# Kernel tuning notes

Measured on AMD Instinct MI355X. Metric: run time of the kernel, lower is better.

## Reference

```python
import jax, jax.numpy as jnp
import numpy as np

B, D_IN, D_HID, NH, PF = 1024, 2048, 4096, 8, 2
D_UP = D_IN * PF          # 4096
HS = D_HID // NH          # 512 head size
EPS = 1e-5


def setup_inputs() -> dict:
    key = jax.random.key(0)
    ks = jax.random.split(key, 24)
    it = iter(range(24))

    def lin(k, fin, fout):
        # weight stored as (in, out); y = x @ W + b
        return jax.random.normal(k, (fin, fout), jnp.float32) / np.float32(np.sqrt(fin))

    def bd(k, fin_blk, fout_blk):
        # block-diagonal per-head weights (NH, in_blk, out_blk)
        return jax.random.normal(k, (NH, fin_blk, fout_blk), jnp.float32) / np.float32(np.sqrt(fin_blk))

    inp = {}
    inp['x'] = jax.random.normal(ks[next(it)], (B, D_IN), jnp.float32)
    inp['h_prev'] = jax.random.normal(ks[next(it)], (B, D_HID), jnp.float32)
    inp['c_prev'] = jax.random.normal(ks[next(it)], (B, D_HID), jnp.float32)
    inp['n_prev'] = jax.random.normal(ks[next(it)], (B, D_HID), jnp.float32)
    inp['m_prev'] = jax.random.normal(ks[next(it)], (B, D_HID), jnp.float32)
    inp['ln_w'] = jnp.ones((D_IN,), jnp.float32)
    inp['ln_b'] = jnp.zeros((D_IN,), jnp.float32)
    inp['upL_w'] = lin(ks[next(it)], D_IN, D_UP); inp['upL_b'] = jnp.zeros((D_UP,), jnp.float32)
    inp['upR_w'] = lin(ks[next(it)], D_IN, D_HID); inp['upR_b'] = jnp.zeros((D_HID,), jnp.float32)
    inp['conv_w'] = jax.random.normal(ks[next(it)], (1, 1, 4), jnp.float32) * 0.5  # (O,I,K)
    inp['conv_b'] = jnp.zeros((1,), jnp.float32)
    inp['skip_w'] = lin(ks[next(it)], D_UP, D_HID); inp['skip_b'] = jnp.zeros((D_HID,), jnp.float32)
    inp['wq'] = bd(ks[next(it)], D_UP // NH, HS); inp['bq'] = jnp.zeros((NH, HS), jnp.float32)
    inp['wk'] = bd(ks[next(it)], D_UP // NH, HS); inp['bk'] = jnp.zeros((NH, HS), jnp.float32)
    inp['wv'] = bd(ks[next(it)], D_UP // NH, HS); inp['bv'] = jnp.zeros((NH, HS), jnp.float32)
    inp['wi_w'] = lin(ks[next(it)], D_UP, D_HID); inp['wi_b'] = jnp.zeros((D_HID,), jnp.float32)
    inp['wf_w'] = lin(ks[next(it)], D_UP, D_HID); inp['wf_b'] = jnp.zeros((D_HID,), jnp.float32)
    inp['wo_w'] = lin(ks[next(it)], D_UP, D_HID); inp['wo_b'] = jnp.zeros((D_HID,), jnp.float32)
    inp['gn_w'] = jnp.ones((D_HID,), jnp.float32)
    inp['gn_b'] = jnp.zeros((D_HID,), jnp.float32)
    inp['down_w'] = lin(ks[next(it)], D_HID, D_IN); inp['down_b'] = jnp.zeros((D_IN,), jnp.float32)
    return inp


def _forward(x, h_prev, c_prev, n_prev, m_prev, ln_w, ln_b, upL_w, upL_b, upR_w, upR_b,
             conv_w, conv_b, skip_w, skip_b, wq, bq, wk, bk, wv, bv,
             wi_w, wi_b, wf_w, wf_b, wo_w, wo_b, gn_w, gn_b, down_w, down_b):
    b = x.shape[0]
    # LayerNorm(input_size)
    mu = jnp.mean(x, axis=-1, keepdims=True)
    var = jnp.var(x, axis=-1, keepdims=True)
    x_norm = (x - mu) * jax.lax.rsqrt(var + EPS) * ln_w + ln_b

    x_up_left = x_norm @ upL_w + upL_b     # (B, D_UP)
    x_up_right = x_norm @ upR_w + upR_b    # (B, D_HID)

    # CausalConv1D(1,1,4): left-pad 3, valid conv  == torch pad 3 both sides + drop last 3
    conv = jax.lax.conv_general_dilated(
        x_up_left[:, None, :], conv_w, window_strides=(1,), padding=((3, 0),),
        dimension_numbers=('NCH', 'OIH', 'NCH'))
    x_conv = jax.nn.silu(conv[:, 0, :] + conv_b[0])   # (B, D_UP)

    x_skip = x_conv @ skip_w + skip_b                 # (B, D_HID)

    def blockdiag(xv, w, bias):
        xh = xv.reshape(b, NH, -1)                    # (B, NH, in_blk)
        return (jnp.einsum('bhi,hio->bho', xh, w) + bias).reshape(b, -1)

    q = blockdiag(x_conv, wq, bq)                                  # (B, D_HID)
    k = blockdiag(x_conv, wk, bk) / np.float32(np.sqrt(HS))
    v = blockdiag(x_up_left, wv, bv)

    i_tilde = x_conv @ wi_w + wi_b
    f_tilde = x_conv @ wf_w + wf_b
    o = jax.nn.sigmoid(x_up_left @ wo_w + wo_b)

    # stabilized exponential gating
    m_t = jnp.maximum(f_tilde + m_prev, i_tilde)
    i_g = jnp.exp(i_tilde - m_t)
    f_g = jnp.exp(f_tilde + m_prev - m_t)
    c_t = f_g * c_prev + i_g * (v * k)
    n_t = f_g * n_prev + i_g * k

    # torch.max(torch.abs(n_t.T @ q), 1)[0] -> (D_HID,)
    denom = jnp.max(jnp.abs(n_t.T @ q), axis=1)
    h_t = o * (c_t * q) / denom                       # broadcast (B,D_HID)/(D_HID,)

    # GroupNorm(NH, D_HID) on 2D input
    hg = h_t.reshape(b, NH, HS)
    mu_g = jnp.mean(hg, axis=-1, keepdims=True)
    var_g = jnp.var(hg, axis=-1, keepdims=True)
    gn = ((hg - mu_g) * jax.lax.rsqrt(var_g + EPS)).reshape(b, D_HID) * gn_w + gn_b

    out = (gn + x_skip) * jax.nn.silu(x_up_right)
    final = out @ down_w + down_b + x
    return final, h_t, c_t, n_t, m_t


def reference(x, h_prev, c_prev, n_prev, m_prev, ln_w, ln_b, upL_w, upL_b, upR_w, upR_b,
              conv_w, conv_b, skip_w, skip_b, wq, bq, wk, bk, wv, bv,
              wi_w, wi_b, wf_w, wf_b, wo_w, wo_b, gn_w, gn_b, down_w, down_b):
    return _forward(x, h_prev, c_prev, n_prev, m_prev, ln_w, ln_b, upL_w, upL_b, upR_w, upR_b,
                    conv_w, conv_b, skip_w, skip_b, wq, bq, wk, bk, wv, bv,
                    wi_w, wi_b, wf_w, wf_b, wo_w, wo_b, gn_w, gn_b, down_w, down_b)
```

## Files before the change

kernel.cpp:

```cpp
#include <hip/hip_runtime.h>
#include <math.h>

#define B_ROWS 1024
#define D_IN   2048
#define D_HID  4096
#define D_UP   4096
#define NH     8
#define HS     512
#define LN_EPS 1e-5f

typedef __attribute__((ext_vector_type(8))) short bf16x8_t;
typedef __attribute__((ext_vector_type(4))) float f32x4_t;
typedef __attribute__((ext_vector_type(4))) unsigned short us4_t;

__device__ __forceinline__ unsigned short f2bf(float f) {
    unsigned int u = __float_as_uint(f);
    u += 0x7fffu + ((u >> 16) & 1u);
    return (unsigned short)(u >> 16);
}
__device__ __forceinline__ float bf2f(unsigned short u) {
    return __uint_as_float(((unsigned int)u) << 16);
}
__device__ __forceinline__ float sigmoidf_(float x) { return 1.0f / (1.0f + expf(-x)); }
__device__ __forceinline__ float siluf_(float x)    { return x / (1.0f + expf(-x)); }

__device__ __forceinline__ void gload16(const unsigned short* g, unsigned short* l) {
    __builtin_amdgcn_global_load_lds(
        (const __attribute__((address_space(1))) unsigned int*)(const void*)g,
        (__attribute__((address_space(3))) unsigned int*)(void*)l,
        16, 0, 0);
}

#define VMW(n) asm volatile("s_waitcnt vmcnt(" #n ")" ::: "memory")

#define XCD_SWZ()                                                        \
    int bx = blockIdx.x, by = blockIdx.y;                                \
    {                                                                    \
        const int gx_ = gridDim.x;                                       \
        const int n_  = gx_ * gridDim.y;                                 \
        if ((n_ & 7) == 0) {                                             \
            int lin = by * gx_ + bx;                                     \
            const int q8 = n_ >> 3;                                      \
            lin = (lin & 7) * q8 + (lin >> 3);                           \
            bx = lin % gx_; by = lin / gx_;                              \
        }                                                                \
    }

struct MGChunk {
    const unsigned short* A;
    const unsigned short* Bt;
    const float* bias;
    const float* resid;
    float* C;
    unsigned short* C2;
    float* denom;
    float alpha;
    int epi;
};

template<int NCH>
__global__ __launch_bounds__(256, 3) void mg256(
    MGChunk c0, MGChunk c1, MGChunk c2, MGChunk c3,
    int K, int lda, int ldbt, int ldc, int bpc,
    long aB, long wB, long bB, long cB)
{
    const int gx = gridDim.x, gy = gridDim.y;
    const int n = gx * gy;
    const int orig = blockIdx.y * gx + blockIdx.x;
    const int wl = ((n & 7) == 0) ? ((orig & 7) * (n >> 3) + (orig >> 3)) : orig;
    const int bxw = wl / gy;
    const int byw = wl - bxw * gy;
    const int chid = (NCH > 1) ? (bxw / bpc) : 0;
    const int cbx = bxw - chid * bpc;
    const MGChunk ch = (chid == 0) ? c0 : ((chid == 1) ? c1 : ((chid == 2) ? c2 : c3));
    const int bz = blockIdx.z;

    const unsigned short* A  = ch.A  + bz * aB;
    const unsigned short* Bt = ch.Bt + bz * wB;

    __shared__ __align__(16) unsigned short As[2][256][32];
    __shared__ __align__(16) unsigned short Bs[2][128][32];

    const int t = threadIdx.x;
    const int w = t >> 6, l = t & 63;
    const int wrm = w >> 1;
    const int wcn = w & 1;
    const long rowA = (long)byw * 256;
    const long rowB = (long)cbx * 128;

    const int skz = (((l & 3) ^ ((l >> 3) & 3)) << 3);
    const unsigned short* Ag = A  + rowA * (long)lda;
    const unsigned short* Bg = Bt + rowB * (long)ldbt;

    const int lm  = l & 15;
    const int pkz = (((l >> 4) ^ ((l >> 1) & 3)) << 3);

    f32x4_t acc[8][4];
#pragma unroll
    for (int mi = 0; mi < 8; ++mi)
#pragma unroll
        for (int ni = 0; ni < 4; ++ni) acc[mi][ni] = (f32x4_t)0.0f;

#define STAGE(buf, kb)                                                        \
    {                                                                         \
        _Pragma("unroll")                                                     \
        for (int p = 0; p < 4; ++p)                                           \
            gload16(Ag + (long)(w * 64 + p * 16 + (l >> 2)) * lda + (kb) + skz, \
                    &As[buf][w * 64 + p * 16][0]);                            \
        _Pragma("unroll")                                                     \
        for (int p = 0; p < 2; ++p)                                           \
            gload16(Bg + (long)(w * 32 + p * 16 + (l >> 2)) * ldbt + (kb) + skz, \
                    &Bs[buf][w * 32 + p * 16][0]);                            \
    }

    const int nsteps = K >> 5;
    STAGE(0, 0);

    int cur = 0;
    for (int ti = 0; ti < nsteps; ++ti) {
        if (ti + 1 < nsteps) {
            STAGE(cur ^ 1, (ti + 1) << 5);
            VMW(6);
        } else {
            VMW(0);
        }
        __builtin_amdgcn_s_barrier();

        bf16x8_t bfr[4];
#pragma unroll
        for (int ni = 0; ni < 4; ++ni)
            bfr[ni] = *(const bf16x8_t*)&Bs[cur][wcn * 64 + ni * 16 + lm][pkz];
#pragma unroll
        for (int mi = 0; mi < 8; ++mi) {
            const bf16x8_t af = *(const bf16x8_t*)&As[cur][wrm * 128 + mi * 16 + lm][pkz];
#pragma unroll
            for (int ni = 0; ni < 4; ++ni)
                acc[mi][ni] = __builtin_amdgcn_mfma_f32_16x16x32_bf16(
                    af, bfr[ni], acc[mi][ni], 0, 0, 0);
        }

        asm volatile("s_waitcnt lgkmcnt(0)" ::: "memory");
        __builtin_amdgcn_s_barrier();
        cur ^= 1;
    }
#undef STAGE

    const int lr4 = (l >> 4) * 4;
    if (ch.epi == 3) {
        float rmax[8][4];
#pragma unroll
        for (int mi = 0; mi < 8; ++mi)
#pragma unroll
            for (int r = 0; r < 4; ++r) {
                float m = 0.0f;
#pragma unroll
                for (int ni = 0; ni < 4; ++ni) m = fmaxf(m, fabsf(acc[mi][ni][r]));
                rmax[mi][r] = m;
            }
#pragma unroll
        for (int off = 1; off < 16; off <<= 1)
#pragma unroll
            for (int mi = 0; mi < 8; ++mi)
#pragma unroll
                for (int r = 0; r < 4; ++r)
                    rmax[mi][r] = fmaxf(rmax[mi][r], __shfl_xor(rmax[mi][r], off, 64));
        if (lm == 0) {
#pragma unroll
            for (int mi = 0; mi < 8; ++mi)
#pragma unroll
                for (int r = 0; r < 4; ++r) {
                    const long m = rowA + wrm * 128 + mi * 16 + lr4 + r;
                    atomicMax((unsigned int*)&ch.denom[m], __float_as_uint(rmax[mi][r]));
                }
        }
        return;
    }
    const float* bias = ch.bias + bz * bB;
#pragma unroll
    for (int mi = 0; mi < 8; ++mi) {
        const long m0 = rowA + wrm * 128 + mi * 16 + lr4;
#pragma unroll
        for (int ni = 0; ni < 4; ++ni) {
            const long nn = rowB + wcn * 64 + ni * 16 + lm;
            const float bv = bias[nn];
#pragma unroll
            for (int r = 0; r < 4; ++r) {
                float v = acc[mi][ni][r] + bv;
                if (ch.epi == 2) v *= ch.alpha;
                const long m = m0 + r;
                if (ch.epi == 5) (ch.C2 + bz * cB)[m * ldc + nn] = f2bf(v);
                else             (ch.C  + bz * cB)[m * ldc + nn] = v;
            }
        }
    }
}

struct MCChunk {
    const unsigned short* A;
    const unsigned short* Bt;
    const float* bias;
    float* C;
    unsigned short* C2;
    float alpha;
    int epi;
};

template<int NCH>
__global__ __launch_bounds__(256) void mgemm_mc(
    MCChunk c0, MCChunk c1, MCChunk c2,
    int K, int lda, int ldbt, int ldc, int bpc,
    long aB, long wB, long bB, long cB)
{
    XCD_SWZ();
    const int chid = bx / bpc;
    const int cbx  = bx - chid * bpc;
    const MCChunk ch = (chid == 0) ? c0 : ((NCH > 1 && chid == 1) ? c1 : c2);
    const int bz = blockIdx.z;

    const unsigned short* A  = ch.A  + bz * aB;
    const unsigned short* Bt = ch.Bt + bz * wB;
    const float* bias = ch.bias + bz * bB;

    __shared__ __align__(16) unsigned short As[2][128][40];
    __shared__ __align__(16) unsigned short Bs[2][128][40];

    const int t = threadIdx.x;
    const int w = t >> 6, l = t & 63;
    const int wr = w >> 1, wc = w & 1;
    const long rowA = (long)by * 128;
    const long rowB = (long)cbx * 128;

    const int lr = t >> 2;
    const int lc = (t & 3) << 3;
    const unsigned short* Ag = A  + (rowA + lr) * (long)lda  + lc;
    const unsigned short* Bg = Bt + (rowB + lr) * (long)ldbt + lc;

    const int lm = l & 15;
    const int lk = (l >> 4) * 8;

    f32x4_t acc[4][4];
#pragma unroll
    for (int mi = 0; mi < 4; ++mi)
#pragma unroll
        for (int ni = 0; ni < 4; ++ni) acc[mi][ni] = (f32x4_t)0.0f;

    bf16x8_t ra[2], rb[2];
#pragma unroll
    for (int p = 0; p < 2; ++p) {
        ra[p] = *(const bf16x8_t*)(Ag + (long)p * 64 * lda);
        rb[p] = *(const bf16x8_t*)(Bg + (long)p * 64 * ldbt);
    }
#pragma unroll
    for (int p = 0; p < 2; ++p) {
        *(bf16x8_t*)&As[0][lr + p * 64][lc] = ra[p];
        *(bf16x8_t*)&Bs[0][lr + p * 64][lc] = rb[p];
    }
    __syncthreads();

    const int nsteps = K >> 5;
    for (int ti = 0; ti < nsteps; ++ti) {
        const int cur = ti & 1;
        if (ti + 1 < nsteps) {
            const int kb = (ti + 1) << 5;
#pragma unroll
            for (int p = 0; p < 2; ++p) {
                ra[p] = *(const bf16x8_t*)(Ag + (long)p * 64 * lda  + kb);
                rb[p] = *(const bf16x8_t*)(Bg + (long)p * 64 * ldbt + kb);
            }
        }
        bf16x8_t af[4], bfr[4];
#pragma unroll
        for (int mi = 0; mi < 4; ++mi)
            af[mi] = *(const bf16x8_t*)&As[cur][wr * 64 + mi * 16 + lm][lk];
#pragma unroll
        for (int ni = 0; ni < 4; ++ni)
            bfr[ni] = *(const bf16x8_t*)&Bs[cur][wc * 64 + ni * 16 + lm][lk];
#pragma unroll
        for (int mi = 0; mi < 4; ++mi)
#pragma unroll
            for (int ni = 0; ni < 4; ++ni)
                acc[mi][ni] = __builtin_amdgcn_mfma_f32_16x16x32_bf16(
                    af[mi], bfr[ni], acc[mi][ni], 0, 0, 0);
        if (ti + 1 < nsteps) {
            const int nxt = cur ^ 1;
#pragma unroll
            for (int p = 0; p < 2; ++p) {
                *(bf16x8_t*)&As[nxt][lr + p * 64][lc] = ra[p];
                *(bf16x8_t*)&Bs[nxt][lr + p * 64][lc] = rb[p];
            }
        }
        __syncthreads();
    }

    const int lr4 = (l >> 4) * 4;
    const float alpha = ch.alpha;
#pragma unroll
    for (int mi = 0; mi < 4; ++mi) {
        const long m0 = rowA + wr * 64 + mi * 16 + lr4;
#pragma unroll
        for (int ni = 0; ni < 4; ++ni) {
            const long nn = rowB + wc * 64 + ni * 16 + lm;
            const float bv = bias[nn];
#pragma unroll
            for (int r = 0; r < 4; ++r) {
                const float v = (acc[mi][ni][r] + bv) * alpha;
                const long m = m0 + r;
                if (ch.epi == 5) (ch.C2 + bz * cB)[m * ldc + nn] = f2bf(v);
                else             (ch.C  + bz * cB)[m * ldc + nn] = v;
            }
        }
    }
}

template<int BM, int EPI>
__global__ __launch_bounds__(256) void mgemm(
    const unsigned short* __restrict__ A, const unsigned short* __restrict__ Bt,
    const float* __restrict__ bias, const float* __restrict__ resid,
    float* __restrict__ C, float* __restrict__ denom,
    int K, int lda, int ldbt, int ldc)
{
    constexpr int MR = BM / 32;
    constexpr int AP = BM / 64;
    XCD_SWZ();

    __shared__ __align__(16) unsigned short As[2][BM][40];
    __shared__ __align__(16) unsigned short Bs[2][128][40];

    const int t = threadIdx.x;
    const int w = t >> 6, l = t & 63;
    const int wr = w >> 1, wc = w & 1;
    const long rowA = (long)by * BM;
    const long rowB = (long)bx * 128;

    const int lr = t >> 2;
    const int lc = (t & 3) << 3;
    const unsigned short* Ag = A  + (rowA + lr) * (long)lda  + lc;
    const unsigned short* Bg = Bt + (rowB + lr) * (long)ldbt + lc;

    const int lm = l & 15;
    const int lk = (l >> 4) * 8;

    f32x4_t acc[MR][4];
#pragma unroll
    for (int mi = 0; mi < MR; ++mi)
#pragma unroll
        for (int ni = 0; ni < 4; ++ni) acc[mi][ni] = (f32x4_t)0.0f;

    bf16x8_t ra[AP], rb[2];
#pragma unroll
    for (int p = 0; p < AP; ++p) ra[p] = *(const bf16x8_t*)(Ag + (long)p * 64 * lda);
#pragma unroll
    for (int p = 0; p < 2;  ++p) rb[p] = *(const bf16x8_t*)(Bg + (long)p * 64 * ldbt);
#pragma unroll
    for (int p = 0; p < AP; ++p) *(bf16x8_t*)&As[0][lr + p * 64][lc] = ra[p];
#pragma unroll
    for (int p = 0; p < 2;  ++p) *(bf16x8_t*)&Bs[0][lr + p * 64][lc] = rb[p];
    __syncthreads();

    const int nsteps = K >> 5;
    for (int ti = 0; ti < nsteps; ++ti) {
        const int cur = ti & 1;
        if (ti + 1 < nsteps) {
            const int kb = (ti + 1) << 5;
#pragma unroll
            for (int p = 0; p < AP; ++p) ra[p] = *(const bf16x8_t*)(Ag + (long)p * 64 * lda  + kb);
#pragma unroll
            for (int p = 0; p < 2;  ++p) rb[p] = *(const bf16x8_t*)(Bg + (long)p * 64 * ldbt + kb);
        }
        bf16x8_t af[MR], bfr[4];
#pragma unroll
        for (int mi = 0; mi < MR; ++mi)
            af[mi] = *(const bf16x8_t*)&As[cur][wr * (BM / 2) + mi * 16 + lm][lk];
#pragma unroll
        for (int ni = 0; ni < 4; ++ni)
            bfr[ni] = *(const bf16x8_t*)&Bs[cur][wc * 64 + ni * 16 + lm][lk];
#pragma unroll
        for (int mi = 0; mi < MR; ++mi)
#pragma unroll
            for (int ni = 0; ni < 4; ++ni)
                acc[mi][ni] = __builtin_amdgcn_mfma_f32_16x16x32_bf16(
                    af[mi], bfr[ni], acc[mi][ni], 0, 0, 0);
        if (ti + 1 < nsteps) {
            const int nxt = cur ^ 1;
#pragma unroll
            for (int p = 0; p < AP; ++p) *(bf16x8_t*)&As[nxt][lr + p * 64][lc] = ra[p];
#pragma unroll
            for (int p = 0; p < 2;  ++p) *(bf16x8_t*)&Bs[nxt][lr + p * 64][lc] = rb[p];
        }
        __syncthreads();
    }

    const int lr4 = (l >> 4) * 4;
#pragma unroll
    for (int mi = 0; mi < MR; ++mi) {
        const long m0 = rowA + wr * (BM / 2) + mi * 16 + lr4;
#pragma unroll
        for (int ni = 0; ni < 4; ++ni) {
            const long nn = rowB + wc * 64 + ni * 16 + lm;
            const float bv = bias[nn];
#pragma unroll
            for (int r = 0; r < 4; ++r) {
                float v = acc[mi][ni][r] + bv;
                const long m = m0 + r;
                if (EPI == 4) v += resid[m * ldc + nn];
                C[m * ldc + nn] = v;
            }
        }
    }
}

struct TP4 {
    const float* s0; const float* s1; const float* s2; const float* s3;
    unsigned short* d0; unsigned short* d1; unsigned short* d2; unsigned short* d3;
};

__global__ __launch_bounds__(256) void tp_batch(TP4 tp, int R, int C)
{
    const int z = blockIdx.z;
    const float* X = (z == 0) ? tp.s0 : (z == 1) ? tp.s1 : (z == 2) ? tp.s2 : tp.s3;
    unsigned short* XT = (z == 0) ? tp.d0 : (z == 1) ? tp.d1 : (z == 2) ? tp.d2 : tp.d3;
    __shared__ float tile[64][65];
    const int t = threadIdx.x;
    const long r0 = (long)blockIdx.y * 64;
    const long c0 = (long)blockIdx.x * 64;
    const int tr = t >> 4;
    const int tc = (t & 15) << 2;
#pragma unroll
    for (int p = 0; p < 4; ++p) {
        const float4 v = *(const float4*)(X + (r0 + tr + p * 16) * C + c0 + tc);
        tile[tr + p * 16][tc + 0] = v.x;
        tile[tr + p * 16][tc + 1] = v.y;
        tile[tr + p * 16][tc + 2] = v.z;
        tile[tr + p * 16][tc + 3] = v.w;
    }
    __syncthreads();
#pragma unroll
    for (int p = 0; p < 2; ++p) {
        const int orow = (t >> 3) + p * 32;
        const int oc8  = (t & 7) * 8;
        unsigned short tmp[8];
#pragma unroll
        for (int j = 0; j < 8; ++j) tmp[j] = f2bf(tile[oc8 + j][orow]);
        *(bf16x8_t*)(XT + (c0 + orow) * (long)R + r0 + oc8) = *(const bf16x8_t*)tmp;
    }
}

__global__ __launch_bounds__(256) void tp_qkv(
    const float* wq, const float* wk, const float* wv, unsigned short* dst)
{
    const int z = blockIdx.z;
    const int sel = z >> 3, head = z & 7;
    const float* X = ((sel == 0) ? wq : (sel == 1) ? wk : wv) + (long)head * HS * HS;
    unsigned short* XT = dst + (long)sel * NH * HS * HS + (long)head * HS * HS;
    __shared__ float tile[64][65];
    const int t = threadIdx.x;
    const long r0 = (long)blockIdx.y * 64;
    const long c0 = (long)blockIdx.x * 64;
    const int tr = t >> 4;
    const int tc = (t & 15) << 2;
#pragma unroll
    for (int p = 0; p < 4; ++p) {
        const float4 v = *(const float4*)(X + (r0 + tr + p * 16) * HS + c0 + tc);
        tile[tr + p * 16][tc + 0] = v.x;
        tile[tr + p * 16][tc + 1] = v.y;
        tile[tr + p * 16][tc + 2] = v.z;
        tile[tr + p * 16][tc + 3] = v.w;
    }
    __syncthreads();
#pragma unroll
    for (int p = 0; p < 2; ++p) {
        const int orow = (t >> 3) + p * 32;
        const int oc8  = (t & 7) * 8;
        unsigned short tmp[8];
#pragma unroll
        for (int j = 0; j < 8; ++j) tmp[j] = f2bf(tile[oc8 + j][orow]);
        *(bf16x8_t*)(XT + (c0 + orow) * (long)HS + r0 + oc8) = *(const bf16x8_t*)tmp;
    }
}

__global__ __launch_bounds__(256) void layernorm_kernel(
    const float* __restrict__ x, const float* __restrict__ w,
    const float* __restrict__ b, unsigned short* __restrict__ out)
{
    __shared__ float sh[8];
    const int row = blockIdx.x, t = threadIdx.x;
    const float* xr = x + (long)row * D_IN;
    float v[8];
    float s = 0.f, ss = 0.f;
#pragma unroll
    for (int i = 0; i < 8; ++i) {
        v[i] = xr[t + 256 * i];
        s += v[i];
        ss += v[i] * v[i];
    }
#pragma unroll
    for (int off = 32; off; off >>= 1) {
        s  += __shfl_down(s, off, 64);
        ss += __shfl_down(ss, off, 64);
    }
    const int lane = t & 63, wid = t >> 6;
    if (lane == 0) { sh[wid * 2] = s; sh[wid * 2 + 1] = ss; }
    __syncthreads();
    s = 0.f; ss = 0.f;
#pragma unroll
    for (int i = 0; i < 4; ++i) { s += sh[i * 2]; ss += sh[i * 2 + 1]; }
    const float mu  = s * (1.0f / D_IN);
    const float var = ss * (1.0f / D_IN) - mu * mu;
    const float rs  = rsqrtf(var + LN_EPS);
    unsigned short* orow = out + (long)row * D_IN;
#pragma unroll
    for (int i = 0; i < 8; ++i) {
        const int d = t + 256 * i;
        orow[d] = f2bf((v[i] - mu) * rs * w[d] + b[d]);
    }
}

__global__ void conv_silu_kernel(const unsigned short* __restrict__ xl,
                                 const float* __restrict__ cw,
                                 const float* __restrict__ cb,
                                 unsigned short* __restrict__ out)
{
    const long idx = (long)blockIdx.x * blockDim.x + threadIdx.x;
    if (idx >= (long)B_ROWS * D_UP) return;
    const int d = (int)(idx & (D_UP - 1));
    const float w0 = cw[0], w1 = cw[1], w2 = cw[2], w3 = cw[3];
    float acc = cb[0] + w3 * bf2f(xl[idx]);
    if (d >= 1) acc += w2 * bf2f(xl[idx - 1]);
    if (d >= 2) acc += w1 * bf2f(xl[idx - 2]);
    if (d >= 3) acc += w0 * bf2f(xl[idx - 3]);
    out[idx] = f2bf(siluf_(acc));
}

__global__ void gating_kernel(const float4* __restrict__ it, const float4* __restrict__ ft,
                              const float4* __restrict__ mp, const float4* __restrict__ cp,
                              const float4* __restrict__ np_, const float4* __restrict__ kk,
                              const float4* __restrict__ vv,
                              float4* __restrict__ mt, float4* __restrict__ ct,
                              float4* __restrict__ nt)
{
    const long idx = (long)blockIdx.x * blockDim.x + threadIdx.x;
    if (idx >= (long)B_ROWS * D_HID / 4) return;
    const float4 i4 = it[idx], f4 = ft[idx], mp4 = mp[idx];
    const float4 cp4 = cp[idx], np4 = np_[idx], k4 = kk[idx], v4 = vv[idx];
    float4 m4, c4, n4;
#pragma unroll
    for (int j = 0; j < 4; ++j) {
        const float i_t = (&i4.x)[j];
        const float f_t = (&f4.x)[j] + (&mp4.x)[j];
        const float m_t = fmaxf(f_t, i_t);
        const float i_g = expf(i_t - m_t);
        const float f_g = expf(f_t - m_t);
        const float kv  = (&k4.x)[j];
        (&c4.x)[j] = f_g * (&cp4.x)[j] + i_g * ((&v4.x)[j] * kv);
        (&n4.x)[j] = f_g * (&np4.x)[j] + i_g * kv;
        (&m4.x)[j] = m_t;
    }
    ct[idx] = c4;
    nt[idx] = n4;
    mt[idx] = m4;
}

__global__ __launch_bounds__(128) void hgnorm_kernel(
    const unsigned short* __restrict__ op, const float* __restrict__ ct,
    const float* __restrict__ qb, const float* __restrict__ denom,
    const float* __restrict__ gw, const float* __restrict__ gb,
    const unsigned short* __restrict__ xskip, const unsigned short* __restrict__ xupR,
    float* __restrict__ ht, unsigned short* __restrict__ out)
{
    __shared__ float sh[4];
    const int b = blockIdx.x >> 3, h = blockIdx.x & 7;
    const int t = threadIdx.x;
    const long base = (long)b * D_HID + h * HS;
    float v[4];
    float s = 0.f, ss = 0.f;
#pragma unroll
    for (int i = 0; i < 4; ++i) {
        const long ix = base + t + 128 * i;
        const int  dg = h * HS + t + 128 * i;
        const float hv = sigmoidf_(bf2f(op[ix])) * ct[ix] * qb[ix] / denom[dg];
        ht[ix] = hv;
        v[i] = hv;
        s += hv;
        ss += hv * hv;
    }
#pragma unroll
    for (int off = 32; off; off >>= 1) {
        s  += __shfl_down(s, off, 64);
        ss += __shfl_down(ss, off, 64);
    }
    if ((t & 63) == 0) { sh[(t >> 6) * 2] = s; sh[(t >> 6) * 2 + 1] = ss; }
    __syncthreads();
    s = sh[0] + sh[2];
    ss = sh[1] + sh[3];
    const float mu  = s * (1.0f / HS);
    const float var = ss * (1.0f / HS) - mu * mu;
    const float rs  = rsqrtf(var + LN_EPS);
#pragma unroll
    for (int i = 0; i < 4; ++i) {
        const int  dg = h * HS + t + 128 * i;
        const long ix = base + t + 128 * i;
        const float g = (v[i] - mu) * rs * gw[dg] + gb[dg];
        out[ix] = f2bf((g + bf2f(xskip[ix])) * siluf_(bf2f(xupR[ix])));
    }
}

extern "C" void kernel_launch(void* const* d_in, const int* in_sizes, int n_in,
                              void* d_out, int out_size, void* d_ws, size_t ws_size,
                              hipStream_t stream)
{
    const float* x      = (const float*)d_in[0];
    const float* c_prev = (const float*)d_in[2];
    const float* n_prev = (const float*)d_in[3];
    const float* m_prev = (const float*)d_in[4];
    const float* ln_w   = (const float*)d_in[5];
    const float* ln_b   = (const float*)d_in[6];
    const float* upL_w  = (const float*)d_in[7];
    const float* upL_b  = (const float*)d_in[8];
    const float* upR_w  = (const float*)d_in[9];
    const float* upR_b  = (const float*)d_in[10];
    const float* conv_w = (const float*)d_in[11];
    const float* conv_b = (const float*)d_in[12];
    const float* skip_w = (const float*)d_in[13];
    const float* skip_b = (const float*)d_in[14];
    const float* wq     = (const float*)d_in[15];
    const float* bq     = (const float*)d_in[16];
    const float* wk     = (const float*)d_in[17];
    const float* bk     = (const float*)d_in[18];
    const float* wv     = (const float*)d_in[19];
    const float* bv     = (const float*)d_in[20];
    const float* wi_w   = (const float*)d_in[21];
    const float* wi_b   = (const float*)d_in[22];
    const float* wf_w   = (const float*)d_in[23];
    const float* wf_b   = (const float*)d_in[24];
    const float* wo_w   = (const float*)d_in[25];
    const float* wo_b   = (const float*)d_in[26];
    const float* gn_w   = (const float*)d_in[27];
    const float* gn_b   = (const float*)d_in[28];
    const float* down_w = (const float*)d_in[29];
    const float* down_b = (const float*)d_in[30];

    float* out     = (float*)d_out;
    float* final_o = out;
    float* ht      = final_o + 2097152;
    float* ct      = ht + 4194304;
    float* nt      = ct + 4194304;
    float* mt      = nt + 4194304;

    unsigned short* WTA = (unsigned short*)ht;
    unsigned short* WTB = (unsigned short*)nt;

    const long M = 1048576;
    float* ws = (float*)d_ws;
    float* qb  = ws +  0 * M;
    float* kb  = ws +  4 * M;
    float* vb  = ws +  8 * M;
    float* itb = ws + 12 * M;
    float* ftb = ws + 16 * M;
    unsigned short* xupR_bf  = (unsigned short*)(ws + 20 * M);
    unsigned short* xskip_bf = (unsigned short*)(ws + 22 * M);
    unsigned short* opb_bf   = (unsigned short*)(ws + 24 * M);
    unsigned short* xnorm_bf = (unsigned short*)(ws + 26 * M);
    unsigned short* xupL_bf  = (unsigned short*)(ws + 27 * M);
    unsigned short* xconv_bf = (unsigned short*)(ws + 29 * M);
    float* denom             = ws + 31 * M;
    unsigned short* WTC      = (unsigned short*)(ws + 32 * M);
    unsigned short* WTD      = (unsigned short*)(ws +  0 * M);
    unsigned short* ntT      = (unsigned short*)(ws + 26 * M);
    unsigned short* qT       = (unsigned short*)(ws + 28 * M);
    unsigned short* dwT      = (unsigned short*)(ws + 12 * M);
    unsigned short* tmp_bf   = (unsigned short*)(ws +  8 * M);

    const float kscale = 1.0f / sqrtf((float)HS);
    const long HS2 = (long)HS * HS;
    MGChunk cz = {};
    MCChunk mz = {};

    layernorm_kernel<<<B_ROWS, 256, 0, stream>>>(x, ln_w, ln_b, xnorm_bf);

    {
        TP4 tp = { upL_w, upR_w, nullptr, nullptr, WTA, WTA + 8388608, nullptr, nullptr };
        tp_batch<<<dim3(64, 32, 2), 256, 0, stream>>>(tp, D_IN, D_UP);
    }
    {
        MCChunk a = { xnorm_bf, WTA,           upL_b, nullptr, xupL_bf, 1.0f, 5 };
        MCChunk b = { xnorm_bf, WTA + 8388608, upR_b, nullptr, xupR_bf, 1.0f, 5 };
        mgemm_mc<2><<<dim3(64, 8, 1), 256, 0, stream>>>(
            a, b, mz, D_IN, D_IN, D_IN, D_HID, 32, 0, 0, 0, 0);
    }

    conv_silu_kernel<<<(B_ROWS * D_UP) / 256, 256, 0, stream>>>(xupL_bf, conv_w, conv_b, xconv_bf);

    {
        TP4 tp = { skip_w, wi_w, wf_w, wo_w, WTA, WTB, WTC, WTD };
        tp_batch<<<dim3(64, 64, 4), 256, 0, stream>>>(tp, D_UP, D_HID);
    }
    {
        MGChunk a = { xconv_bf, WTA, skip_b, nullptr, nullptr, xskip_bf, nullptr, 1.0f, 5 };
        MGChunk b = { xconv_bf, WTB, wi_b,   nullptr, itb,     nullptr,  nullptr, 1.0f, 0 };
        MGChunk c = { xconv_bf, WTC, wf_b,   nullptr, ftb,     nullptr,  nullptr, 1.0f, 0 };
        MGChunk d = { xupL_bf,  WTD, wo_b,   nullptr, nullptr, opb_bf,   nullptr, 1.0f, 5 };
        mg256<4><<<dim3(128, 4, 1), 256, 0, stream>>>(
            a, b, c, d, D_UP, D_UP, D_UP, D_HID, 32, 0, 0, 0, 0);
    }

    tp_qkv<<<dim3(8, 8, 24), 256, 0, stream>>>(wq, wk, wv, WTA);
    {
        MCChunk a = { xconv_bf, WTA,                bq, qb, nullptr, 1.0f,   0 };
        MCChunk b = { xconv_bf, WTA + NH * HS2,     bk, kb, nullptr, kscale, 0 };
        MCChunk c = { xupL_bf,  WTA + 2 * NH * HS2, bv, vb, nullptr, 1.0f,   0 };
        mgemm_mc<3><<<dim3(12, 8, NH), 256, 0, stream>>>(
            a, b, c, HS, D_UP, HS, D_HID, 4, HS, HS2, HS, HS);
    }

    gating_kernel<<<(B_ROWS * D_HID / 4) / 256, 256, 0, stream>>>(
        (const float4*)itb, (const float4*)ftb, (const float4*)m_prev,
        (const float4*)c_prev, (const float4*)n_prev, (const float4*)kb,
        (const float4*)vb, (float4*)mt, (float4*)ct, (float4*)nt);

    {
        TP4 tp = { nt, qb, nullptr, nullptr, ntT, qT, nullptr, nullptr };
        tp_batch<<<dim3(64, 16, 2), 256, 0, stream>>>(tp, B_ROWS, D_HID);
    }
    hipMemsetAsync(denom, 0, D_HID * sizeof(float), stream);
    {
        MGChunk a = { ntT, qT, nullptr, nullptr, nullptr, nullptr, denom, 1.0f, 3 };
        mg256<1><<<dim3(32, 16, 1), 256, 0, stream>>>(
            a, cz, cz, cz, B_ROWS, B_ROWS, B_ROWS, 0, 32, 0, 0, 0, 0);
    }

    {
        TP4 tp = { down_w, nullptr, nullptr, nullptr, dwT, nullptr, nullptr, nullptr };
        tp_batch<<<dim3(32, 64, 1), 256, 0, stream>>>(tp, D_HID, D_IN);
    }

    hgnorm_kernel<<<B_ROWS * NH, 128, 0, stream>>>(
        opb_bf, ct, qb, denom, gn_w, gn_b, xskip_bf, xupR_bf, ht, tmp_bf);

    mgemm<64, 4><<<dim3(16, 16, 1), 256, 0, stream>>>(
        tmp_bf, dwT, down_b, x, final_o, nullptr, D_HID, D_HID, D_HID, D_IN);
}
```

Before: 555.9 us.

## Fuse weight transpose and bf16 conversion into GEMM B-tile loading

Removes the separate transpose/convert kernels for all weight matrices and the q transpose. The GEMM kernels now read fp32 row-major weights directly from global memory, convert them to bf16 in registers and write them transposed into shared memory. This drops several full passes over large weight tensors and their launches. The cost is strided scalar fp32 loads and per-element conversion inside the inner loop, more register pressure, and B loads that are no longer asynchronous direct-to-LDS, which could hurt the main GEMMs.

```diff
diff --git a/kernel.cpp b/kernel.cpp
--- a/kernel.cpp
+++ b/kernel.cpp
@@ -48,9 +48,8 @@
 
 struct MGChunk {
     const unsigned short* A;
-    const unsigned short* Bt;
+    const float* Wf;
     const float* bias;
-    const float* resid;
     float* C;
     unsigned short* C2;
     float* denom;
@@ -61,7 +60,7 @@
 template<int NCH>
 __global__ __launch_bounds__(256, 3) void mg256(
     MGChunk c0, MGChunk c1, MGChunk c2, MGChunk c3,
-    int K, int lda, int ldbt, int ldc, int bpc,
+    int K, int lda, int ldw, int ldc, int bpc,
     long aB, long wB, long bB, long cB)
 {
     const int gx = gridDim.x, gy = gridDim.y;
@@ -76,10 +75,10 @@
     const int bz = blockIdx.z;
 
     const unsigned short* A  = ch.A  + bz * aB;
-    const unsigned short* Bt = ch.Bt + bz * wB;
+    const float*          Wf = ch.Wf + bz * wB;
 
     __shared__ __align__(16) unsigned short As[2][256][32];
-    __shared__ __align__(16) unsigned short Bs[2][128][32];
+    __shared__ __align__(16) unsigned short Bs[2][128][40];
 
     const int t = threadIdx.x;
     const int w = t >> 6, l = t & 63;
@@ -89,10 +88,14 @@
     const long rowB = (long)cbx * 128;
 
     const int skz = (((l & 3) ^ ((l >> 3) & 3)) << 3);
-    const unsigned short* Ag = A  + rowA * (long)lda;
-    const unsigned short* Bg = Bt + rowB * (long)ldbt;
+    const unsigned short* Ag = A + rowA * (long)lda;
+
+    const int nB = t & 127;
+    const int k0 = (t >> 7) * 8;
+    const float* Wg = Wf + rowB + nB;
 
     const int lm  = l & 15;
+    const int lk  = (l >> 4) * 8;
     const int pkz = (((l >> 4) ^ ((l >> 1) & 3)) << 3);
 
     f32x4_t acc[8][4];
@@ -101,26 +104,50 @@
 #pragma unroll
         for (int ni = 0; ni < 4; ++ni) acc[mi][ni] = (f32x4_t)0.0f;
 
-#define STAGE(buf, kb)                                                        \
+    float rbf[2][8];
+
+#define LOADB(kb)                                                             \
+    {                                                                         \
+        _Pragma("unroll")                                                     \
+        for (int q = 0; q < 2; ++q)                                           \
+            _Pragma("unroll")                                                 \
+            for (int j = 0; j < 8; ++j)                                       \
+                rbf[q][j] = Wg[(long)((kb) + k0 + q * 16 + j) * ldw];         \
+    }
+#define WRITEB(buf)                                                           \
+    {                                                                         \
+        _Pragma("unroll")                                                     \
+        for (int q = 0; q < 2; ++q) {                                         \
+            unsigned short tmpw[8];                                           \
+            _Pragma("unroll")                                                 \
+            for (int j = 0; j < 8; ++j) tmpw[j] = f2bf(rbf[q][j]);            \
+            *(bf16x8_t*)&Bs[buf][nB][k0 + q * 16] = *(const bf16x8_t*)tmpw;   \
+        }                                                                     \
+    }
+#define STAGEA(buf, kb)                                                       \
     {                                                                         \
         _Pragma("unroll")                                                     \
         for (int p = 0; p < 4; ++p)                                           \
             gload16(Ag + (long)(w * 64 + p * 16 + (l >> 2)) * lda + (kb) + skz, \
                     &As[buf][w * 64 + p * 16][0]);                            \
-        _Pragma("unroll")                                                     \
-        for (int p = 0; p < 2; ++p)                                           \
-            gload16(Bg + (long)(w * 32 + p * 16 + (l >> 2)) * ldbt + (kb) + skz, \
-                    &Bs[buf][w * 32 + p * 16][0]);                            \
     }
 
     const int nsteps = K >> 5;
-    STAGE(0, 0);
+    LOADB(0);
+    STAGEA(0, 0);
+    WRITEB(0);
+    VMW(0);
+    asm volatile("s_waitcnt lgkmcnt(0)" ::: "memory");
+    __builtin_amdgcn_s_barrier();
 
     int cur = 0;
     for (int ti = 0; ti < nsteps; ++ti) {
-        if (ti + 1 < nsteps) {
-            STAGE(cur ^ 1, (ti + 1) << 5);
-            VMW(6);
+        const bool pf = (ti + 1 < nsteps);
+        if (pf) {
+            const int kb1 = (ti + 1) << 5;
+            LOADB(kb1);
+            STAGEA(cur ^ 1, kb1);
+            VMW(20);
         } else {
             VMW(0);
         }
@@ -129,7 +156,7 @@
         bf16x8_t bfr[4];
 #pragma unroll
         for (int ni = 0; ni < 4; ++ni)
-            bfr[ni] = *(const bf16x8_t*)&Bs[cur][wcn * 64 + ni * 16 + lm][pkz];
+            bfr[ni] = *(const bf16x8_t*)&Bs[cur][wcn * 64 + ni * 16 + lm][lk];
 #pragma unroll
         for (int mi = 0; mi < 8; ++mi) {
             const bf16x8_t af = *(const bf16x8_t*)&As[cur][wrm * 128 + mi * 16 + lm][pkz];
@@ -139,11 +166,14 @@
                     af, bfr[ni], acc[mi][ni], 0, 0, 0);
         }
 
+        if (pf) WRITEB(cur ^ 1);
         asm volatile("s_waitcnt lgkmcnt(0)" ::: "memory");
         __builtin_amdgcn_s_barrier();
         cur ^= 1;
     }
-#undef STAGE
+#undef LOADB
+#undef WRITEB
+#undef STAGEA
 
     const int lr4 = (l >> 4) * 4;
     if (ch.epi == 3) {
@@ -197,7 +227,7 @@
 
 struct MCChunk {
     const unsigned short* A;
-    const unsigned short* Bt;
+    const float* Wf;
     const float* bias;
     float* C;
     unsigned short* C2;
@@ -208,7 +238,7 @@
 template<int NCH>
 __global__ __launch_bounds__(256) void mgemm_mc(
     MCChunk c0, MCChunk c1, MCChunk c2,
-    int K, int lda, int ldbt, int ldc, int bpc,
+    int K, int lda, int ldw, int ldc, int bpc,
     long aB, long wB, long bB, long cB)
 {
     XCD_SWZ();
@@ -218,7 +248,7 @@
     const int bz = blockIdx.z;
 
     const unsigned short* A  = ch.A  + bz * aB;
-    const unsigned short* Bt = ch.Bt + bz * wB;
+    const float*          Wf = ch.Wf + bz * wB;
     const float* bias = ch.bias + bz * bB;
 
     __shared__ __align__(16) unsigned short As[2][128][40];
@@ -232,10 +262,13 @@
 
     const int lr = t >> 2;
     const int lc = (t & 3) << 3;
-    const unsigned short* Ag = A  + (rowA + lr) * (long)lda  + lc;
-    const unsigned short* Bg = Bt + (rowB + lr) * (long)ldbt + lc;
-
-    const int lm = l & 15;
+    const unsigned short* Ag = A + (rowA + lr) * (long)lda + lc;
+
+    const int nB = t & 127;
+    const int k0 = (t >> 7) * 8;
+    const float* Wg = Wf + rowB + nB;
+
+    const int lm = t & 15 ? (l & 15) : (l & 15);
     const int lk = (l >> 4) * 8;
 
     f32x4_t acc[4][4];
@@ -244,16 +277,24 @@
 #pragma unroll
         for (int ni = 0; ni < 4; ++ni) acc[mi][ni] = (f32x4_t)0.0f;
 
-    bf16x8_t ra[2], rb[2];
-#pragma unroll
-    for (int p = 0; p < 2; ++p) {
-        ra[p] = *(const bf16x8_t*)(Ag + (long)p * 64 * lda);
-        rb[p] = *(const bf16x8_t*)(Bg + (long)p * 64 * ldbt);
-    }
-#pragma unroll
-    for (int p = 0; p < 2; ++p) {
-        *(bf16x8_t*)&As[0][lr + p * 64][lc] = ra[p];
-        *(bf16x8_t*)&Bs[0][lr + p * 64][lc] = rb[p];
+    bf16x8_t ra[2];
+    float rbf[2][8];
+
+#pragma unroll
+    for (int p = 0; p < 2; ++p) ra[p] = *(const bf16x8_t*)(Ag + (long)p * 64 * lda);
+#pragma unroll
+    for (int q = 0; q < 2; ++q)
+#pragma unroll
+        for (int j = 0; j < 8; ++j)
+            rbf[q][j] = Wg[(long)(k0 + q * 16 + j) * ldw];
+#pragma unroll
+    for (int p = 0; p < 2; ++p) *(bf16x8_t*)&As[0][lr + p * 64][lc] = ra[p];
+#pragma unroll
+    for (int q = 0; q < 2; ++q) {
+        unsigned short tmpw[8];
+#pragma unroll
+        for (int j = 0; j < 8; ++j) tmpw[j] = f2bf(rbf[q][j]);
+        *(bf16x8_t*)&Bs[0][nB][k0 + q * 16] = *(const bf16x8_t*)tmpw;
     }
     __syncthreads();
 
@@ -263,18 +304,21 @@
         if (ti + 1 < nsteps) {
             const int kb = (ti + 1) << 5;
 #pragma unroll
-            for (int p = 0; p < 2; ++p) {
-                ra[p] = *(const bf16x8_t*)(Ag + (long)p * 64 * lda  + kb);
-                rb[p] = *(const bf16x8_t*)(Bg + (long)p * 64 * ldbt + kb);
-            }
+            for (int p = 0; p < 2; ++p)
+                ra[p] = *(const bf16x8_t*)(Ag + (long)p * 64 * lda + kb);
+#pragma unroll
+            for (int q = 0; q < 2; ++q)
+#pragma unroll
+                for (int j = 0; j < 8; ++j)
+                    rbf[q][j] = Wg[(long)(kb + k0 + q * 16 + j) * ldw];
         }
         bf16x8_t af[4], bfr[4];
 #pragma unroll
         for (int mi = 0; mi < 4; ++mi)
-            af[mi] = *(const bf16x8_t*)&As[cur][wr * 64 + mi * 16 + lm][lk];
+            af[mi] = *(const bf16x8_t*)&As[cur][wr * 64 + mi * 16 + (l & 15)][lk];
 #pragma unroll
         for (int ni = 0; ni < 4; ++ni)
-            bfr[ni] = *(const bf16x8_t*)&Bs[cur][wc * 64 + ni * 16 + lm][lk];
+            bfr[ni] = *(const bf16x8_t*)&Bs[cur][wc * 64 + ni * 16 + (l & 15)][lk];
 #pragma unroll
         for (int mi = 0; mi < 4; ++mi)
 #pragma unroll
@@ -284,9 +328,14 @@
         if (ti + 1 < nsteps) {
             const int nxt = cur ^ 1;
 #pragma unroll
-            for (int p = 0; p < 2; ++p) {
+            for (int p = 0; p < 2; ++p)
                 *(bf16x8_t*)&As[nxt][lr + p * 64][lc] = ra[p];
-                *(bf16x8_t*)&Bs[nxt][lr + p * 64][lc] = rb[p];
+#pragma unroll
+            for (int q = 0; q < 2; ++q) {
+                unsigned short tmpw[8];
+#pragma unroll
+                for (int j = 0; j < 8; ++j) tmpw[j] = f2bf(rbf[q][j]);
+                *(bf16x8_t*)&Bs[nxt][nB][k0 + q * 16] = *(const bf16x8_t*)tmpw;
             }
         }
         __syncthreads();
@@ -299,7 +348,7 @@
         const long m0 = rowA + wr * 64 + mi * 16 + lr4;
 #pragma unroll
         for (int ni = 0; ni < 4; ++ni) {
-            const long nn = rowB + wc * 64 + ni * 16 + lm;
+            const long nn = rowB + wc * 64 + ni * 16 + (l & 15);
             const float bv = bias[nn];
 #pragma unroll
             for (int r = 0; r < 4; ++r) {
@@ -314,10 +363,10 @@
 
 template<int BM, int EPI>
 __global__ __launch_bounds__(256) void mgemm(
-    const unsigned short* __restrict__ A, const unsigned short* __restrict__ Bt,
+    const unsigned short* __restrict__ A, const float* __restrict__ Wf,
     const float* __restrict__ bias, const float* __restrict__ resid,
-    float* __restrict__ C, float* __restrict__ denom,
-    int K, int lda, int ldbt, int ldc)
+    float* __restrict__ C,
+    int K, int lda, int ldw, int ldc)
 {
     constexpr int MR = BM / 32;
     constexpr int AP = BM / 64;
@@ -334,8 +383,11 @@
 
     const int lr = t >> 2;
     const int lc = (t & 3) << 3;
-    const unsigned short* Ag = A  + (rowA + lr) * (long)lda  + lc;
-    const unsigned short* Bg = Bt + (rowB + lr) * (long)ldbt + lc;
+    const unsigned short* Ag = A + (rowA + (lr & (BM - 1))) * (long)lda + lc;
+
+    const int nB = t & 127;
+    const int k0 = (t >> 7) * 8;
+    const float* Wg = Wf + rowB + nB;
 
     const int lm = l & 15;
     const int lk = (l >> 4) * 8;
@@ -346,15 +398,27 @@
 #pragma unroll
         for (int ni = 0; ni < 4; ++ni) acc[mi][ni] = (f32x4_t)0.0f;
 
-    bf16x8_t ra[AP], rb[2];
+    bf16x8_t ra[AP];
+    float rbf[2][8];
+
 #pragma unroll
     for (int p = 0; p < AP; ++p) ra[p] = *(const bf16x8_t*)(Ag + (long)p * 64 * lda);
 #pragma unroll
-    for (int p = 0; p < 2;  ++p) rb[p] = *(const bf16x8_t*)(Bg + (long)p * 64 * ldbt);
-#pragma unroll
-    for (int p = 0; p < AP; ++p) *(bf16x8_t*)&As[0][lr + p * 64][lc] = ra[p];
-#pragma unroll
-    for (int p = 0; p < 2;  ++p) *(bf16x8_t*)&Bs[0][lr + p * 64][lc] = rb[p];
+    for (int q = 0; q < 2; ++q)
+#pragma unroll
+        for (int j = 0; j < 8; ++j)
+            rbf[q][j] = Wg[(long)(k0 + q * 16 + j) * ldw];
+    if (lr < BM) {
+#pragma unroll
+        for (int p = 0; p < AP; ++p) *(bf16x8_t*)&As[0][(lr & (BM - 1)) + p * 64][lc] = ra[p];
+    }
+#pragma unroll
+    for (int q = 0; q < 2; ++q) {
+        unsigned short tmpw[8];
+#pragma unroll
+        for (int j = 0; j < 8; ++j) tmpw[j] = f2bf(rbf[q][j]);
+        *(bf16x8_t*)&Bs[0][nB][k0 + q * 16] = *(const bf16x8_t*)tmpw;
+    }
     __syncthreads();
 
     const int nsteps = K >> 5;
@@ -363,9 +427,13 @@
         if (ti + 1 < nsteps) {
             const int kb = (ti + 1) << 5;
 #pragma unroll
-            for (int p = 0; p < AP; ++p) ra[p] = *(const bf16x8_t*)(Ag + (long)p * 64 * lda  + kb);
-#pragma unroll
-            for (int p = 0; p < 2;  ++p) rb[p] = *(const bf16x8_t*)(Bg + (long)p * 64 * ldbt + kb);
+            for (int p = 0; p < AP; ++p)
+                ra[p] = *(const bf16x8_t*)(Ag + (long)p * 64 * lda + kb);
+#pragma unroll
+            for (int q = 0; q < 2; ++q)
+#pragma unroll
+                for (int j = 0; j < 8; ++j)
+                    rbf[q][j] = Wg[(long)(kb + k0 + q * 16 + j) * ldw];
         }
         bf16x8_t af[MR], bfr[4];
 #pragma unroll
@@ -382,10 +450,18 @@
                     af[mi], bfr[ni], acc[mi][ni], 0, 0, 0);
         if (ti + 1 < nsteps) {
             const int nxt = cur ^ 1;
-#pragma unroll
-            for (int p = 0; p < AP; ++p) *(bf16x8_t*)&As[nxt][lr + p * 64][lc] = ra[p];
-#pragma unroll
-            for (int p = 0; p < 2;  ++p) *(bf16x8_t*)&Bs[nxt][lr + p * 64][lc] = rb[p];
+            if (lr < BM) {
+#pragma unroll
+                for (int p = 0; p < AP; ++p)
+                    *(bf16x8_t*)&As[nxt][(lr & (BM - 1)) + p * 64][lc] = ra[p];
+            }
+#pragma unroll
+            for (int q = 0; q < 2; ++q) {
+                unsigned short tmpw[8];
+#pragma unroll
+                for (int j = 0; j < 8; ++j) tmpw[j] = f2bf(rbf[q][j]);
+                *(bf16x8_t*)&Bs[nxt][nB][k0 + q * 16] = *(const bf16x8_t*)tmpw;
+            }
         }
         __syncthreads();
     }
@@ -442,39 +518,6 @@
 #pragma unroll
         for (int j = 0; j < 8; ++j) tmp[j] = f2bf(tile[oc8 + j][orow]);
         *(bf16x8_t*)(XT + (c0 + orow) * (long)R + r0 + oc8) = *(const bf16x8_t*)tmp;
-    }
-}
-
-__global__ __launch_bounds__(256) void tp_qkv(
-    const float* wq, const float* wk, const float* wv, unsigned short* dst)
-{
-    const int z = blockIdx.z;
-    const int sel = z >> 3, head = z & 7;
-    const float* X = ((sel == 0) ? wq : (sel == 1) ? wk : wv) + (long)head * HS * HS;
-    unsigned short* XT = dst + (long)sel * NH * HS * HS + (long)head * HS * HS;
-    __shared__ float tile[64][65];
-    const int t = threadIdx.x;
-    const long r0 = (long)blockIdx.y * 64;
-    const long c0 = (long)blockIdx.x * 64;
-    const int tr = t >> 4;
-    const int tc = (t & 15) << 2;
-#pragma unroll
-    for (int p = 0; p < 4; ++p) {
-        const float4 v = *(const float4*)(X + (r0 + tr + p * 16) * HS + c0 + tc);
-        tile[tr + p * 16][tc + 0] = v.x;
-        tile[tr + p * 16][tc + 1] = v.y;
-        tile[tr + p * 16][tc + 2] = v.z;
-        tile[tr + p * 16][tc + 3] = v.w;
-    }
-    __syncthreads();
-#pragma unroll
-    for (int p = 0; p < 2; ++p) {
-        const int orow = (t >> 3) + p * 32;
-        const int oc8  = (t & 7) * 8;
-        unsigned short tmp[8];
-#pragma unroll
-        for (int j = 0; j < 8; ++j) tmp[j] = f2bf(tile[oc8 + j][orow]);
-        *(bf16x8_t*)(XT + (c0 + orow) * (long)HS + r0 + oc8) = *(const bf16x8_t*)tmp;
     }
 }
 
@@ -646,9 +689,6 @@
     float* nt      = ct + 4194304;
     float* mt      = nt + 4194304;
 
-    unsigned short* WTA = (unsigned short*)ht;
-    unsigned short* WTB = (unsigned short*)nt;
-
     const long M = 1048576;
     float* ws = (float*)d_ws;
     float* qb  = ws +  0 * M;
@@ -663,11 +703,7 @@
     unsigned short* xupL_bf  = (unsigned short*)(ws + 27 * M);
     unsigned short* xconv_bf = (unsigned short*)(ws + 29 * M);
     float* denom             = ws + 31 * M;
-    unsigned short* WTC      = (unsigned short*)(ws + 32 * M);
-    unsigned short* WTD      = (unsigned short*)(ws +  0 * M);
     unsigned short* ntT      = (unsigned short*)(ws + 26 * M);
-    unsigned short* qT       = (unsigned short*)(ws + 28 * M);
-    unsigned short* dwT      = (unsigned short*)(ws + 12 * M);
     unsigned short* tmp_bf   = (unsigned short*)(ws +  8 * M);
 
     const float kscale = 1.0f / sqrtf((float)HS);
@@ -678,36 +714,27 @@
     layernorm_kernel<<<B_ROWS, 256, 0, stream>>>(x, ln_w, ln_b, xnorm_bf);
 
     {
-        TP4 tp = { upL_w, upR_w, nullptr, nullptr, WTA, WTA + 8388608, nullptr, nullptr };
-        tp_batch<<<dim3(64, 32, 2), 256, 0, stream>>>(tp, D_IN, D_UP);
-    }
+        MCChunk a = { xnorm_bf, upL_w, upL_b, nullptr, xupL_bf, 1.0f, 5 };
+        MCChunk b = { xnorm_bf, upR_w, upR_b, nullptr, xupR_bf, 1.0f, 5 };
+        mgemm_mc<2><<<dim3(64, 8, 1), 256, 0, stream>>>(
+            a, b, mz, D_IN, D_IN, D_UP, D_HID, 32, 0, 0, 0, 0);
+    }
+
+    conv_silu_kernel<<<(B_ROWS * D_UP) / 256, 256, 0, stream>>>(xupL_bf, conv_w, conv_b, xconv_bf);
+
     {
-        MCChunk a = { xnorm_bf, WTA,           upL_b, nullptr, xupL_bf, 1.0f, 5 };
-        MCChunk b = { xnorm_bf, WTA + 8388608, upR_b, nullptr, xupR_bf, 1.0f, 5 };
-        mgemm_mc<2><<<dim3(64, 8, 1), 256, 0, stream>>>(
-            a, b, mz, D_IN, D_IN, D_IN, D_HID, 32, 0, 0, 0, 0);
-    }
-
-    conv_silu_kernel<<<(B_ROWS * D_UP) / 256, 256, 0, stream>>>(xupL_bf, conv_w, conv_b, xconv_bf);
+        MGChunk a = { xconv_bf, skip_w, skip_b, nullptr, xskip_bf, nullptr, 1.0f, 5 };
+        MGChunk b = { xconv_bf, wi_w,   wi_b,   itb,     nullptr,  nullptr, 1.0f, 0 };
+        MGChunk c = { xconv_bf, wf_w,   wf_b,   ftb,     nullptr,  nullptr, 1.0f, 0 };
+        MGChunk d = { xupL_bf,  wo_w,   wo_b,   nullptr, opb_bf,   nullptr, 1.0f, 5 };
+        mg256<4><<<dim3(128, 4, 1), 256, 0, stream>>>(
+            a, b, c, d, D_UP, D_UP, D_HID, D_HID, 32, 0, 0, 0, 0);
+    }
 
     {
-        TP4 tp = { skip_w, wi_w, wf_w, wo_w, WTA, WTB, WTC, WTD };
-        tp_batch<<<dim3(64, 64, 4), 256, 0, stream>>>(tp, D_UP, D_HID);
-    }
-    {
-        MGChunk a = { xconv_bf, WTA, skip_b, nullptr, nullptr, xskip_bf, nullptr, 1.0f, 5 };
-        MGChunk b = { xconv_bf, WTB, wi_b,   nullptr, itb,     nullptr,  nullptr, 1.0f, 0 };
-        MGChunk c = { xconv_bf, WTC, wf_b,   nullptr, ftb,     nullptr,  nullptr, 1.0f, 0 };
-        MGChunk d = { xupL_bf,  WTD, wo_b,   nullptr, nullptr, opb_bf,   nullptr, 1.0f, 5 };
-        mg256<4><<<dim3(128, 4, 1), 256, 0, stream>>>(
-            a, b, c, d, D_UP, D_UP, D_UP, D_HID, 32, 0, 0, 0, 0);
-    }
-
-    tp_qkv<<<dim3(8, 8, 24), 256, 0, stream>>>(wq, wk, wv, WTA);
-    {
-        MCChunk a = { xconv_bf, WTA,                bq, qb, nullptr, 1.0f,   0 };
-        MCChunk b = { xconv_bf, WTA + NH * HS2,     bk, kb, nullptr, kscale, 0 };
-        MCChunk c = { xupL_bf,  WTA + 2 * NH * HS2, bv, vb, nullptr, 1.0f,   0 };
+        MCChunk a = { xconv_bf, wq, bq, qb, nullptr, 1.0f,   0 };
+        MCChunk b = { xconv_bf, wk, bk, kb, nullptr, kscale, 0 };
+        MCChunk c = { xupL_bf,  wv, bv, vb, nullptr, 1.0f,   0 };
         mgemm_mc<3><<<dim3(12, 8, NH), 256, 0, stream>>>(
             a, b, c, HS, D_UP, HS, D_HID, 4, HS, HS2, HS, HS);
     }
@@ -718,24 +745,19 @@
         (const float4*)vb, (float4*)mt, (float4*)ct, (float4*)nt);
 
     {
-        TP4 tp = { nt, qb, nullptr, nullptr, ntT, qT, nullptr, nullptr };
-        tp_batch<<<dim3(64, 16, 2), 256, 0, stream>>>(tp, B_ROWS, D_HID);
+        TP4 tp = { nt, nullptr, nullptr, nullptr, ntT, nullptr, nullptr, nullptr };
+        tp_batch<<<dim3(64, 16, 1), 256, 0, stream>>>(tp, B_ROWS, D_HID);
     }
     hipMemsetAsync(denom, 0, D_HID * sizeof(float), stream);
     {
-        MGChunk a = { ntT, qT, nullptr, nullptr, nullptr, nullptr, denom, 1.0f, 3 };
+        MGChunk a = { ntT, qb, nullptr, nullptr, nullptr, denom, 1.0f, 3 };
         mg256<1><<<dim3(32, 16, 1), 256, 0, stream>>>(
-            a, cz, cz, cz, B_ROWS, B_ROWS, B_ROWS, 0, 32, 0, 0, 0, 0);
-    }
-
-    {
-        TP4 tp = { down_w, nullptr, nullptr, nullptr, dwT, nullptr, nullptr, nullptr };
-        tp_batch<<<dim3(32, 64, 1), 256, 0, stream>>>(tp, D_HID, D_IN);
+            a, cz, cz, cz, B_ROWS, B_ROWS, D_HID, 0, 32, 0, 0, 0, 0);
     }
 
     hgnorm_kernel<<<B_ROWS * NH, 128, 0, stream>>>(
         opb_bf, ct, qb, denom, gn_w, gn_b, xskip_bf, xupR_bf, ht, tmp_bf);
 
     mgemm<64, 4><<<dim3(16, 16, 1), 256, 0, stream>>>(
-        tmp_bf, dwT, down_b, x, final_o, nullptr, D_HID, D_HID, D_HID, D_IN);
-}
+        tmp_bf, down_w, down_b, x, final_o, D_HID, D_HID, D_IN, D_IN);
+}
```

Result: slower. 1.689 ms (+203.8%).
